# Optimization experiments

Hardware: AMD Instinct MI355X
Metric: run time of the kernel (lower is better)

## Reference

```python
import jax, jax.numpy as jnp
import numpy as np

N_CLASS = 20
N_SIGMA = 2
H = W = 512
B = 4
N_INST = 32
W_INST, W_VAR, W_SEED = 1.0, 10.0, 1.0
FG_WEIGHT = 10.0


def _xym():
    # channel 0: x along width, channel 1: y along height (matches torch buffer)
    xm = jnp.broadcast_to(jnp.linspace(0.0, 1.0, W)[None, :], (H, W))
    ym = jnp.broadcast_to(jnp.linspace(0.0, 1.0, H)[:, None], (H, W))
    return jnp.stack([xm, ym], axis=0)  # [2, H, W]


def lovasz_hinge_flat(logits, gt, valid):
    # logits, gt (0/1 float), valid (bool), all flat [P]; ignored pixels excluded
    P = logits.shape[0]
    vf = valid.astype(logits.dtype)
    signs = 2.0 * gt - 1.0
    # push ignored pixels to the end of the descending sort; relu(-1e9)=0 kills them
    errors = jnp.where(valid, 1.0 - logits * signs, -1e9)
    errors_sorted, perm = jax.lax.top_k(errors, P)  # descending
    gt_sorted = jnp.take(gt * vf, perm)
    v_sorted = jnp.take(vf, perm)
    gts = jnp.sum(gt * vf)
    inter = gts - jnp.cumsum(gt_sorted)
    union = gts + jnp.cumsum((1.0 - gt_sorted) * v_sorted)
    jac = 1.0 - inter / jnp.maximum(union, 1e-9)
    jac = jnp.concatenate([jac[:1], jac[1:] - jac[:-1]])
    return jnp.sum(jax.nn.relu(errors_sorted) * jac)


def _per_image(pred_b, inst_b, lab_b, xym, fg_w, n_inst):
    spatial_emb = jnp.tanh(pred_b[:2]) + xym            # [2,H,W]
    sigma = pred_b[2:2 + N_SIGMA]                       # [n_sigma,H,W]
    seed = jax.nn.sigmoid(pred_b[2 + N_SIGMA:2 + N_SIGMA + N_CLASS])  # [C,H,W]
    inst = inst_b[0]
    lab = lab_b[0]
    valid = (lab != 255)

    # background seed loss: sum over classes of seed^2 on pixels not of that class
    cls_ids = jnp.arange(N_CLASS)
    bg = (lab[None] != (cls_ids + 1)[:, None, None]) & valid[None]
    seed_bg = jnp.sum(jnp.square(seed) * bg)

    def per_inst(iid):
        m = (inst == iid)
        mf = m.astype(pred_b.dtype)
        cnt = jnp.maximum(jnp.sum(mf), 1.0)
        # to_center=True: center is mean coordinate of instance pixels
        center = jnp.sum(xym * mf[None], axis=(1, 2)) / cnt          # [2]
        s_mean = jnp.sum(sigma * mf[None], axis=(1, 2)) / cnt        # [n_sigma]
        var_l = jnp.sum(jnp.square(sigma - jax.lax.stop_gradient(s_mean)[:, None, None]) * mf[None]) / (N_SIGMA * cnt)
        s = jnp.exp(s_mean * 10.0)
        dist = jnp.exp(-jnp.sum(jnp.square(spatial_emb - center[:, None, None]) * s[:, None, None], axis=0))  # [H,W]
        inst_l = lovasz_hinge_flat((dist * 2.0 - 1.0).reshape(-1), mf.reshape(-1), valid.reshape(-1))
        cls = jnp.max(lab * m) - 1  # instance class (0-indexed)
        seed_c = jnp.take(seed, cls, axis=0)
        seed_fg = jnp.take(fg_w, cls) * jnp.sum(jnp.square(seed_c - jax.lax.stop_gradient(dist)) * mf)
        return inst_l, var_l, seed_fg

    inst_ls, var_ls, seed_fgs = jax.vmap(per_inst)(jnp.arange(1, n_inst + 1))
    instance_loss = jnp.sum(inst_ls) / n_inst
    var_loss = jnp.sum(var_ls) / n_inst
    seed_loss = (seed_bg + jnp.sum(seed_fgs)) / (H * W)
    return W_INST * instance_loss + W_VAR * var_loss + W_SEED * seed_loss


def setup_inputs() -> dict:
    key = jax.random.key(0)
    k1, k2 = jax.random.split(key)
    prediction = jax.random.normal(k1, (B, 2 + N_SIGMA + N_CLASS, H, W), dtype=jnp.float32)
    instances = jax.random.randint(k2, (B, 1, H, W), 0, N_INST + 1).astype(jnp.int32)
    # each instance id has a consistent class, as the torch instance_to_cls dict assumes
    labels = jnp.where(instances > 0, ((instances - 1) % N_CLASS) + 1, 0).astype(jnp.int32)
    return {"prediction": prediction, "instances": instances, "labels": labels, "n_instances": N_INST}


def reference(prediction, instances, labels, n_instances):
    xym = _xym()
    fg_w = jnp.full((N_CLASS,), FG_WEIGHT, dtype=prediction.dtype)
    per = jax.vmap(lambda p, i, l: _per_image(p, i, l, xym, fg_w, n_instances))(prediction, instances, labels)
    return jnp.mean(per) + jnp.sum(prediction) * 0.0
```

## Files before the change

kernel.cpp:

```cpp
#include <hip/hip_runtime.h>
#include <hip/hip_fp16.h>
#include <math.h>

#define HH 512
#define WW 512
#define BB 4
#define NCLS 20
#define NINST 32
#define NPIX (HH*WW)
#define NCH 24
#define NBIN 128
#define NCHUNK3 256
#define CPX3 1024
#define K3T 512
#define HSTR 33

#define OFF_PARTA  ((size_t)0)
#define OFF_PSEED  (OFF_PARTA + 1024*256*4)
#define OFF_STATS  (OFF_PSEED + 1024*8)
#define OFF_SEEDBG (OFF_STATS + 8*128*4)
#define OFF_VALID  (OFF_SEEDBG + 4*4)
#define OFF_INSTL  (OFF_VALID + 4*4)
#define OFF_SFG    (OFF_INSTL + 128*4)
#define OFF_REC    ((OFF_SFG + 1024*4 + 255) & ~(size_t)255)
#define OFF_HIST   (OFF_REC + (size_t)BB*NPIX*8)

__device__ __forceinline__ float fast_rcp(float x) { return __builtin_amdgcn_rcpf(x); }
__device__ __forceinline__ float fast_sigmoid(float z) { return fast_rcp(1.0f + __expf(-z)); }
__device__ __forceinline__ float fast_tanh(float x) {
  return 1.0f - 2.0f * fast_rcp(__expf(2.0f * x) + 1.0f);
}

__global__ __launch_bounds__(256) void k1_stats(
    const float* __restrict__ pred, const int* __restrict__ inst,
    const int* __restrict__ lab,
    float* __restrict__ partA, float2* __restrict__ partSeed,
    uint2* __restrict__ rec)
{
  __shared__ unsigned s_st[4][NINST][9];
  __shared__ float s_seed, s_valid;
  int t = threadIdx.x;
  int w = t >> 6;
  for (int i = t; i < 4*NINST*9; i += 256) ((unsigned*)s_st)[i] = 0u;
  if (t == 0) { s_seed = 0.f; s_valid = 0.f; }
  __syncthreads();

  int b = blockIdx.x >> 8;
  int p = (blockIdx.x & 255) * 1024 + t * 4;
  const float* pb = pred + (size_t)b*NCH*NPIX;

  float4 e0v = *(const float4*)(pb + p);
  float4 e1v = *(const float4*)(pb + NPIX + p);
  float4 g0v = *(const float4*)(pb + 2*NPIX + p);
  float4 g1v = *(const float4*)(pb + 3*NPIX + p);
  int4 idv = *(const int4*)(inst + (size_t)b*NPIX + p);
  int4 lbv = *(const int4*)(lab + (size_t)b*NPIX + p);
  float4 sv[12];
  #pragma unroll
  for (int c = 0; c < 12; ++c) sv[c] = *(const float4*)(pb + (size_t)(4+c)*NPIX + p);

  #pragma unroll
  for (int u = 0; u < 4; ++u) {
    int px = p + u;
    int x = px & (WW-1);
    int y = px >> 9;
    float xm = x * (1.0f/(WW-1));
    float ym = y * (1.0f/(HH-1));
    float g0 = (&g0v.x)[u];
    float g1 = (&g1v.x)[u];
    int id = (&idv.x)[u];
    int lb = (&lbv.x)[u];
    if (id >= 1) {
      int j = id - 1;
      unsigned* row = s_st[w][j];
      atomicAdd(&row[0], 1u | ((lb != 255) ? 0x10000u : 0u));
      atomicAdd((float*)&row[1], xm);
      atomicAdd((float*)&row[2], ym);
      atomicAdd((float*)&row[3], g0);
      atomicAdd((float*)&row[4], g1);
      atomicAdd((float*)&row[5], g0*g0);
      atomicAdd((float*)&row[6], g1*g1);
    }
  }

  float4 sv2[8];
  #pragma unroll
  for (int c = 0; c < 8; ++c) sv2[c] = *(const float4*)(pb + (size_t)(16+c)*NPIX + p);

  float so[4] = {0.f,0.f,0.f,0.f};
  float Sv[4] = {0.f,0.f,0.f,0.f};
  #pragma unroll
  for (int c = 0; c < 12; ++c) {
    #pragma unroll
    for (int u = 0; u < 4; ++u) {
      float sg = fast_sigmoid((&sv[c].x)[u]);
      Sv[u] += sg*sg;
      if (c + 1 == (&lbv.x)[u]) so[u] = sg;
    }
  }
  #pragma unroll
  for (int c = 0; c < 8; ++c) {
    #pragma unroll
    for (int u = 0; u < 4; ++u) {
      float sg = fast_sigmoid((&sv2[c].x)[u]);
      Sv[u] += sg*sg;
      if (c + 13 == (&lbv.x)[u]) so[u] = sg;
    }
  }
  float seedloc = 0.f, vloc = 0.f;
  #pragma unroll
  for (int u = 0; u < 4; ++u)
    if ((&lbv.x)[u] != 255) { seedloc += Sv[u] - so[u]*so[u]; vloc += 1.0f; }

  {
    uint2 r4[4];
    #pragma unroll
    for (int u = 0; u < 4; ++u) {
      int px = p + u;
      int x = px & (WW-1);
      int y = px >> 9;
      float ex = fast_tanh((&e0v.x)[u]) + x * (1.0f/(WW-1));
      float ey = fast_tanh((&e1v.x)[u]) + y * (1.0f/(HH-1));
      __half2 h = __floats2half2_rn(ex, ey);
      unsigned valid = ((&lbv.x)[u] != 255) ? 1u : 0u;
      unsigned meta = (unsigned)(&idv.x)[u] | (valid << 7);
      r4[u].x = *reinterpret_cast<unsigned*>(&h);
      r4[u].y = (unsigned)(unsigned char)(so[u]*255.f + 0.5f) | (meta << 8);
    }
    uint4* dst = (uint4*)(rec + (size_t)b*NPIX + p);
    dst[0] = make_uint4(r4[0].x, r4[0].y, r4[1].x, r4[1].y);
    dst[1] = make_uint4(r4[2].x, r4[2].y, r4[3].x, r4[3].y);
  }
  for (int o = 32; o; o >>= 1) {
    seedloc += __shfl_down(seedloc, o);
    vloc    += __shfl_down(vloc, o);
  }
  if ((t & 63) == 0) { atomicAdd(&s_seed, seedloc); atomicAdd(&s_valid, vloc); }
  __syncthreads();

  {
    int j = t & 31, f = t >> 5;
    float v;
    if (f == 0) {
      unsigned s = (s_st[0][j][0] & 0xFFFFu) + (s_st[1][j][0] & 0xFFFFu)
                 + (s_st[2][j][0] & 0xFFFFu) + (s_st[3][j][0] & 0xFFFFu);
      v = (float)s;
    } else if (f == 7) {
      unsigned s = (s_st[0][j][0] >> 16) + (s_st[1][j][0] >> 16)
                 + (s_st[2][j][0] >> 16) + (s_st[3][j][0] >> 16);
      v = (float)s;
    } else {
      v = __uint_as_float(s_st[0][j][f]) + __uint_as_float(s_st[1][j][f])
        + __uint_as_float(s_st[2][j][f]) + __uint_as_float(s_st[3][j][f]);
    }
    partA[(blockIdx.x << 8) + t] = v;
  }
  if (t == 0) partSeed[blockIdx.x] = make_float2(s_seed, s_valid);
}

__global__ __launch_bounds__(256) void k2a_reduce(
    const float* __restrict__ partA, const float2* __restrict__ partSeed,
    float* __restrict__ stats, float* __restrict__ seedbg,
    float* __restrict__ validT)
{
  int bid = blockIdx.x;
  int t = threadIdx.x;
  if (bid < 32) {
    __shared__ float red[256];
    int b = bid >> 3, f = bid & 7;
    int j = t & 31, grp = t >> 5;
    float s = 0.f;
    #pragma unroll 8
    for (int k = 0; k < 32; ++k)
      s += partA[((b*256 + grp*32 + k) << 8) + (f << 5) + j];
    red[t] = s; __syncthreads();
    for (int st = 128; st >= 32; st >>= 1) {
      if (t < st) red[t] += red[t + st];
      __syncthreads();
    }
    if (t < 32) stats[f*128 + b*32 + t] = red[t];
  } else {
    int img = t >> 6, slot = t & 63;
    float s = 0.f, v = 0.f;
    #pragma unroll
    for (int k = 0; k < 4; ++k) {
      float2 ps = partSeed[img*256 + slot*4 + k];
      s += ps.x; v += ps.y;
    }
    for (int o = 32; o; o >>= 1) {
      s += __shfl_down(s, o);
      v += __shfl_down(v, o);
    }
    if (slot == 0) { seedbg[img] = s; validT[img] = v; }
  }
}

__global__ __launch_bounds__(K3T) void k3_hist(
    const uint2* __restrict__ rec, const float* __restrict__ stats,
    unsigned* __restrict__ hist, float* __restrict__ sfg)
{
  __shared__ unsigned hc[NBIN*HSTR];
  __shared__ float sder[NINST][4];
  __shared__ float s_fg[8];
  int t = threadIdx.x;
  int bid = blockIdx.x;
  int b = bid >> 8;
  int chunk = bid & 255;
  for (int i = t; i < NBIN*HSTR; i += K3T) hc[i] = 0u;
  if (t < NINST) {
    int pr = b*NINST + t;
    float cnt = fmaxf(stats[0*128+pr], 1.0f);
    float rc = fast_rcp(cnt);
    sder[t][0] = stats[1*128+pr] * rc;
    sder[t][1] = stats[2*128+pr] * rc;
    sder[t][2] = -1.442695041f * __expf(10.f * stats[3*128+pr] * rc);
    sder[t][3] = -1.442695041f * __expf(10.f * stats[4*128+pr] * rc);
  }
  __syncthreads();

  int w = t >> 6, lane = t & 63;
  int j = lane & 31, jp1 = j + 1;
  float cx = sder[j][0], cy = sder[j][1];
  float s0 = sder[j][2], s1 = sder[j][3];
  const uint2* rb = rec + (size_t)b*NPIX + chunk*CPX3 + w*128;

  float fg = 0.f;
  #pragma unroll 4
  for (int r = 0; r < 64; ++r) {
    uint2 rv = rb[r*2 + (lane >> 5)];
    __half2 h;
    *reinterpret_cast<unsigned*>(&h) = rv.x;
    float2 e = __half22float2(h);
    unsigned hi = rv.y;
    float dx = e.x - cx, dy = e.y - cy;
    float dist = exp2f(dx*dx*s0 + dy*dy*s1);
    bool own = ((int)((hi >> 8) & 0x3F) == jp1);
    if (own) { float d = (float)(hi & 0xFFu)*(1.0f/255.f) - dist; fg += d*d; }
    if (hi & 0x8000u) {
      float f = own ? (1.0f - dist) : dist;
      unsigned bin = min((unsigned)(f * (float)NBIN), NBIN-1u);
      if (bin) atomicAdd(&hc[bin*HSTR + j], own ? 0x10001u : 1u);
    }
  }
  for (int o = 32; o; o >>= 1) fg += __shfl_down(fg, o);
  if (lane == 0) s_fg[w] = fg;
  __syncthreads();
  if (t == 0) {
    float s = 0.f;
    #pragma unroll
    for (int i = 0; i < 8; ++i) s += s_fg[i];
    sfg[bid] = 10.0f * s;
  }
  unsigned* out = hist + (size_t)(b*NCHUNK3 + chunk) * (NINST*NBIN);
  #pragma unroll
  for (int k = 0; k < NINST*NBIN/K3T; ++k) {
    int idx = k*K3T + t;
    out[idx] = hc[(idx & 127)*HSTR + (idx >> 7)];
  }
}

__global__ __launch_bounds__(512) void k4_scan(
    const unsigned* __restrict__ hist, const float* __restrict__ stats,
    const float* __restrict__ validT, float* __restrict__ instl)
{
  __shared__ unsigned s_c[4][NBIN], s_p[4][NBIN];
  __shared__ unsigned rc[NBIN], rp[NBIN];
  int t = threadIdx.x;
  int pair = blockIdx.x;
  int b = pair >> 5, j = pair & 31;
  int grp = t >> 7, bin = t & 127;
  const unsigned* bp = hist + ((size_t)b*NCHUNK3*NINST + j)*NBIN + bin;
  unsigned c = 0, p = 0;
  #pragma unroll 8
  for (int ch = grp*64; ch < grp*64 + 64; ++ch) {
    unsigned v = bp[(size_t)ch * (NINST*NBIN)];
    c += v & 0xFFFFu; p += v >> 16;
  }
  s_c[grp][bin] = c; s_p[grp][bin] = p;
  __syncthreads();
  if (t < NBIN) {
    unsigned cc = s_c[0][t] + s_c[1][t] + s_c[2][t] + s_c[3][t];
    unsigned pp = s_p[0][t] + s_p[1][t] + s_p[2][t] + s_p[3][t];
    s_c[0][t] = cc; s_p[0][t] = pp;
    rc[t] = t ? cc : 0u; rp[t] = t ? pp : 0u;
  }
  __syncthreads();
  for (int st = 64; st; st >>= 1) {
    if (t < st) { rc[t] += rc[t+st]; rp[t] += rp[t+st]; }
    __syncthreads();
  }
  float G = stats[7*128+pair];
  if (t == 0) {
    s_c[0][0] = (unsigned)validT[b] - rc[0];
    s_p[0][0] = (unsigned)G - rp[0];
  }
  __syncthreads();

  if (t < 64) {
    int lane = t;
    unsigned carryN = 0, carryP = 0;
    float Jprev = 0.f, L = 0.f;
    for (int c8 = 0; c8 < NBIN/64; ++c8) {
      int k = NBIN - 1 - c8*64 - lane;
      unsigned n = s_c[0][k], pp0 = s_p[0][k];
      for (int off = 1; off < 64; off <<= 1) {
        unsigned nn = __shfl_up(n, off);
        unsigned pq = __shfl_up(pp0, off);
        if (lane >= off) { n += nn; pp0 += pq; }
      }
      float fN = (float)(carryN + n);
      float fP = (float)(carryP + pp0);
      float uni = G + fN - fP;
      float J = 1.0f - (G - fP) / fmaxf(uni, 1e-9f);
      float Jp = __shfl_up(J, 1);
      if (lane == 0) Jp = Jprev;
      float v = (k + 0.5f) * (2.0f/NBIN);
      L += v * (J - Jp);
      carryN += __shfl(n, 63);
      carryP += __shfl(pp0, 63);
      Jprev  = __shfl(J, 63);
    }
    for (int o = 32; o; o >>= 1) L += __shfl_down(L, o);
    if (lane == 0) instl[pair] = L;
  }
}

__global__ __launch_bounds__(512) void k5_final(
    const float* __restrict__ instl, const float* __restrict__ stats,
    const float* __restrict__ seedbg, const float* __restrict__ sfg,
    float* __restrict__ out)
{
  __shared__ float red[512];
  int t = threadIdx.x;
  float acc = (sfg[t] + sfg[t + 512]) * (1.0f/NPIX);
  if (t < 4) acc += seedbg[t] * (1.0f/NPIX);
  if (t < 128) {
    float cntA = stats[0*128+t];
    float cnt = fmaxf(cntA, 1.0f);
    float s0 = stats[3*128+t], s1 = stats[4*128+t];
    float q0 = stats[5*128+t], q1 = stats[6*128+t];
    float sm0 = s0/cnt, sm1 = s1/cnt;
    float varnum = q0 - 2.f*sm0*s0 + cntA*sm0*sm0
                 + q1 - 2.f*sm1*s1 + cntA*sm1*sm1;
    float varl = varnum / (2.0f * cnt);
    acc += (instl[t] + 10.0f*varl) * (1.0f/NINST);
  }
  red[t] = acc; __syncthreads();
  for (int st = 256; st; st >>= 1) {
    if (t < st) red[t] += red[t+st];
    __syncthreads();
  }
  if (t == 0) out[0] = red[0] * (1.0f/BB);
}

extern "C" void kernel_launch(void* const* d_in, const int* in_sizes, int n_in,
                              void* d_out, int out_size, void* d_ws, size_t ws_size,
                              hipStream_t stream)
{
  const float* pred = (const float*)d_in[0];
  const int* inst = (const int*)d_in[1];
  const int* lab  = (const int*)d_in[2];
  char* ws = (char*)d_ws;
  float* partA = (float*)(ws + OFF_PARTA);
  float2* partSeed = (float2*)(ws + OFF_PSEED);
  float* stats = (float*)(ws + OFF_STATS);
  float* seedbg = (float*)(ws + OFF_SEEDBG);
  float* validT = (float*)(ws + OFF_VALID);
  float* instl = (float*)(ws + OFF_INSTL);
  float* sfg = (float*)(ws + OFF_SFG);
  uint2* rec = (uint2*)(ws + OFF_REC);
  unsigned* hist = (unsigned*)(ws + OFF_HIST);

  hipLaunchKernelGGL(k1_stats, dim3(1024), dim3(256), 0, stream,
                     pred, inst, lab, partA, partSeed, rec);
  hipLaunchKernelGGL(k2a_reduce, dim3(33), dim3(256), 0, stream,
                     partA, partSeed, stats, seedbg, validT);
  hipLaunchKernelGGL(k3_hist, dim3(BB*NCHUNK3), dim3(K3T), 0, stream,
                     rec, stats, hist, sfg);
  hipLaunchKernelGGL(k4_scan, dim3(128), dim3(512), 0, stream,
                     hist, stats, validT, instl);
  hipLaunchKernelGGL(k5_final, dim3(1), dim3(512), 0, stream,
                     instl, stats, seedbg, sfg, (float*)d_out);
}
```

Measured before the change: 91.79 us.

## Halve per-thread pixels in stats kernel and fuse final reduction into scan

The stats kernel now launches 2048 blocks with two pixels per thread instead of 1024 blocks with four. Seed channels are streamed in a loop rather than held as 20 float4 registers, which lowers register pressure and raises occupancy. The final single-block kernel is removed: each scan block adds its instance and variance terms to the output atomically, and block 0 also adds the seed terms. The output is zeroed in the first kernel, and float atomic accumulation makes the summation order nondeterministic.

New measurement: 89.05 us. -3.0%, faster.

```diff
diff --git a/kernel.cpp b/kernel.cpp
--- a/kernel.cpp
+++ b/kernel.cpp
@@ -16,12 +16,11 @@
 #define HSTR 33
 
 #define OFF_PARTA  ((size_t)0)
-#define OFF_PSEED  (OFF_PARTA + 1024*256*4)
-#define OFF_STATS  (OFF_PSEED + 1024*8)
+#define OFF_PSEED  (OFF_PARTA + 2048*256*4)
+#define OFF_STATS  (OFF_PSEED + 2048*8)
 #define OFF_SEEDBG (OFF_STATS + 8*128*4)
 #define OFF_VALID  (OFF_SEEDBG + 4*4)
-#define OFF_INSTL  (OFF_VALID + 4*4)
-#define OFF_SFG    (OFF_INSTL + 128*4)
+#define OFF_SFG    (OFF_VALID + 4*4)
 #define OFF_REC    ((OFF_SFG + 1024*4 + 255) & ~(size_t)255)
 #define OFF_HIST   (OFF_REC + (size_t)BB*NPIX*8)
 
@@ -35,7 +34,7 @@
     const float* __restrict__ pred, const int* __restrict__ inst,
     const int* __restrict__ lab,
     float* __restrict__ partA, float2* __restrict__ partSeed,
-    uint2* __restrict__ rec)
+    uint2* __restrict__ rec, float* __restrict__ outz)
 {
   __shared__ unsigned s_st[4][NINST][9];
   __shared__ float s_seed, s_valid;
@@ -43,24 +42,21 @@
   int w = t >> 6;
   for (int i = t; i < 4*NINST*9; i += 256) ((unsigned*)s_st)[i] = 0u;
   if (t == 0) { s_seed = 0.f; s_valid = 0.f; }
-  __syncthreads();
-
-  int b = blockIdx.x >> 8;
-  int p = (blockIdx.x & 255) * 1024 + t * 4;
+  if (blockIdx.x == 0 && t == 0) outz[0] = 0.f;
+  __syncthreads();
+
+  int b = blockIdx.x >> 9;
+  int p = (blockIdx.x & 511) * 512 + t * 2;
   const float* pb = pred + (size_t)b*NCH*NPIX;
-
-  float4 e0v = *(const float4*)(pb + p);
-  float4 e1v = *(const float4*)(pb + NPIX + p);
-  float4 g0v = *(const float4*)(pb + 2*NPIX + p);
-  float4 g1v = *(const float4*)(pb + 3*NPIX + p);
-  int4 idv = *(const int4*)(inst + (size_t)b*NPIX + p);
-  int4 lbv = *(const int4*)(lab + (size_t)b*NPIX + p);
-  float4 sv[12];
+  float2 e0v = *(const float2*)(pb + p);
+  float2 e1v = *(const float2*)(pb + NPIX + p);
+  float2 g0v = *(const float2*)(pb + 2*NPIX + p);
+  float2 g1v = *(const float2*)(pb + 3*NPIX + p);
+  int2 idv = *(const int2*)(inst + (size_t)b*NPIX + p);
+  int2 lbv = *(const int2*)(lab + (size_t)b*NPIX + p);
+
   #pragma unroll
-  for (int c = 0; c < 12; ++c) sv[c] = *(const float4*)(pb + (size_t)(4+c)*NPIX + p);
-
-  #pragma unroll
-  for (int u = 0; u < 4; ++u) {
+  for (int u = 0; u < 2; ++u) {
     int px = p + u;
     int x = px & (WW-1);
     int y = px >> 9;
@@ -83,53 +79,37 @@
     }
   }
 
-  float4 sv2[8];
-  #pragma unroll
-  for (int c = 0; c < 8; ++c) sv2[c] = *(const float4*)(pb + (size_t)(16+c)*NPIX + p);
-
-  float so[4] = {0.f,0.f,0.f,0.f};
-  float Sv[4] = {0.f,0.f,0.f,0.f};
-  #pragma unroll
-  for (int c = 0; c < 12; ++c) {
+  float so0 = 0.f, so1 = 0.f, Sv0 = 0.f, Sv1 = 0.f;
+  for (int c = 0; c < NCLS; ++c) {
+    float2 sv = *(const float2*)(pb + (size_t)(4+c)*NPIX + p);
+    float sg0 = fast_sigmoid(sv.x);
+    float sg1 = fast_sigmoid(sv.y);
+    Sv0 += sg0*sg0;
+    Sv1 += sg1*sg1;
+    if (c + 1 == lbv.x) so0 = sg0;
+    if (c + 1 == lbv.y) so1 = sg1;
+  }
+  float seedloc = 0.f, vloc = 0.f;
+  if (lbv.x != 255) { seedloc += Sv0 - so0*so0; vloc += 1.0f; }
+  if (lbv.y != 255) { seedloc += Sv1 - so1*so1; vloc += 1.0f; }
+
+  {
+    uint2 r4[2];
     #pragma unroll
-    for (int u = 0; u < 4; ++u) {
-      float sg = fast_sigmoid((&sv[c].x)[u]);
-      Sv[u] += sg*sg;
-      if (c + 1 == (&lbv.x)[u]) so[u] = sg;
-    }
-  }
-  #pragma unroll
-  for (int c = 0; c < 8; ++c) {
-    #pragma unroll
-    for (int u = 0; u < 4; ++u) {
-      float sg = fast_sigmoid((&sv2[c].x)[u]);
-      Sv[u] += sg*sg;
-      if (c + 13 == (&lbv.x)[u]) so[u] = sg;
-    }
-  }
-  float seedloc = 0.f, vloc = 0.f;
-  #pragma unroll
-  for (int u = 0; u < 4; ++u)
-    if ((&lbv.x)[u] != 255) { seedloc += Sv[u] - so[u]*so[u]; vloc += 1.0f; }
-
-  {
-    uint2 r4[4];
-    #pragma unroll
-    for (int u = 0; u < 4; ++u) {
+    for (int u = 0; u < 2; ++u) {
       int px = p + u;
       int x = px & (WW-1);
       int y = px >> 9;
       float ex = fast_tanh((&e0v.x)[u]) + x * (1.0f/(WW-1));
       float ey = fast_tanh((&e1v.x)[u]) + y * (1.0f/(HH-1));
       __half2 h = __floats2half2_rn(ex, ey);
-      unsigned valid = ((&lbv.x)[u] != 255) ? 1u : 0u;
+      unsigned valid = (((&lbv.x)[u]) != 255) ? 1u : 0u;
       unsigned meta = (unsigned)(&idv.x)[u] | (valid << 7);
+      float sou = u ? so1 : so0;
       r4[u].x = *reinterpret_cast<unsigned*>(&h);
-      r4[u].y = (unsigned)(unsigned char)(so[u]*255.f + 0.5f) | (meta << 8);
-    }
-    uint4* dst = (uint4*)(rec + (size_t)b*NPIX + p);
-    dst[0] = make_uint4(r4[0].x, r4[0].y, r4[1].x, r4[1].y);
-    dst[1] = make_uint4(r4[2].x, r4[2].y, r4[3].x, r4[3].y);
+      r4[u].y = (unsigned)(unsigned char)(sou*255.f + 0.5f) | (meta << 8);
+    }
+    *(uint4*)(rec + (size_t)b*NPIX + p) = make_uint4(r4[0].x, r4[0].y, r4[1].x, r4[1].y);
   }
   for (int o = 32; o; o >>= 1) {
     seedloc += __shfl_down(seedloc, o);
@@ -171,8 +151,8 @@
     int j = t & 31, grp = t >> 5;
     float s = 0.f;
     #pragma unroll 8
-    for (int k = 0; k < 32; ++k)
-      s += partA[((b*256 + grp*32 + k) << 8) + (f << 5) + j];
+    for (int k = 0; k < 64; ++k)
+      s += partA[((b*512 + grp*64 + k) << 8) + (f << 5) + j];
     red[t] = s; __syncthreads();
     for (int st = 128; st >= 32; st >>= 1) {
       if (t < st) red[t] += red[t + st];
@@ -183,8 +163,8 @@
     int img = t >> 6, slot = t & 63;
     float s = 0.f, v = 0.f;
     #pragma unroll
-    for (int k = 0; k < 4; ++k) {
-      float2 ps = partSeed[img*256 + slot*4 + k];
+    for (int k = 0; k < 8; ++k) {
+      float2 ps = partSeed[img*512 + slot*8 + k];
       s += ps.x; v += ps.y;
     }
     for (int o = 32; o; o >>= 1) {
@@ -259,12 +239,14 @@
   }
 }
 
-__global__ __launch_bounds__(512) void k4_scan(
+__global__ __launch_bounds__(512) void k4_final(
     const unsigned* __restrict__ hist, const float* __restrict__ stats,
-    const float* __restrict__ validT, float* __restrict__ instl)
+    const float* __restrict__ validT, const float* __restrict__ seedbg,
+    const float* __restrict__ sfg, float* __restrict__ out)
 {
   __shared__ unsigned s_c[4][NBIN], s_p[4][NBIN];
   __shared__ unsigned rc[NBIN], rp[NBIN];
+  __shared__ float s_L;
   int t = threadIdx.x;
   int pair = blockIdx.x;
   int b = pair >> 5, j = pair & 31;
@@ -321,36 +303,31 @@
       Jprev  = __shfl(J, 63);
     }
     for (int o = 32; o; o >>= 1) L += __shfl_down(L, o);
-    if (lane == 0) instl[pair] = L;
-  }
-}
-
-__global__ __launch_bounds__(512) void k5_final(
-    const float* __restrict__ instl, const float* __restrict__ stats,
-    const float* __restrict__ seedbg, const float* __restrict__ sfg,
-    float* __restrict__ out)
-{
-  __shared__ float red[512];
-  int t = threadIdx.x;
-  float acc = (sfg[t] + sfg[t + 512]) * (1.0f/NPIX);
-  if (t < 4) acc += seedbg[t] * (1.0f/NPIX);
-  if (t < 128) {
-    float cntA = stats[0*128+t];
+    if (lane == 0) s_L = L;
+  }
+  __syncthreads();
+  if (t == 0) {
+    float cntA = stats[0*128+pair];
     float cnt = fmaxf(cntA, 1.0f);
-    float s0 = stats[3*128+t], s1 = stats[4*128+t];
-    float q0 = stats[5*128+t], q1 = stats[6*128+t];
+    float s0 = stats[3*128+pair], s1 = stats[4*128+pair];
+    float q0 = stats[5*128+pair], q1 = stats[6*128+pair];
     float sm0 = s0/cnt, sm1 = s1/cnt;
     float varnum = q0 - 2.f*sm0*s0 + cntA*sm0*sm0
                  + q1 - 2.f*sm1*s1 + cntA*sm1*sm1;
     float varl = varnum / (2.0f * cnt);
-    acc += (instl[t] + 10.0f*varl) * (1.0f/NINST);
-  }
-  red[t] = acc; __syncthreads();
-  for (int st = 256; st; st >>= 1) {
-    if (t < st) red[t] += red[t+st];
-    __syncthreads();
-  }
-  if (t == 0) out[0] = red[0] * (1.0f/BB);
+    atomicAdd(out, (s_L + 10.0f*varl) * (1.0f/(NINST*BB)));
+  }
+  if (pair == 0) {
+    __shared__ float red[512];
+    float acc = sfg[t] + sfg[t + 512];
+    if (t < 4) acc += seedbg[t];
+    red[t] = acc; __syncthreads();
+    for (int st = 256; st; st >>= 1) {
+      if (t < st) red[t] += red[t+st];
+      __syncthreads();
+    }
+    if (t == 0) atomicAdd(out, red[0] * (1.0f/((float)NPIX*BB)));
+  }
 }
 
 extern "C" void kernel_launch(void* const* d_in, const int* in_sizes, int n_in,
@@ -366,19 +343,16 @@
   float* stats = (float*)(ws + OFF_STATS);
   float* seedbg = (float*)(ws + OFF_SEEDBG);
   float* validT = (float*)(ws + OFF_VALID);
-  float* instl = (float*)(ws + OFF_INSTL);
   float* sfg = (float*)(ws + OFF_SFG);
   uint2* rec = (uint2*)(ws + OFF_REC);
   unsigned* hist = (unsigned*)(ws + OFF_HIST);
 
-  hipLaunchKernelGGL(k1_stats, dim3(1024), dim3(256), 0, stream,
-                     pred, inst, lab, partA, partSeed, rec);
+  hipLaunchKernelGGL(k1_stats, dim3(2048), dim3(256), 0, stream,
+                     pred, inst, lab, partA, partSeed, rec, (float*)d_out);
   hipLaunchKernelGGL(k2a_reduce, dim3(33), dim3(256), 0, stream,
                      partA, partSeed, stats, seedbg, validT);
   hipLaunchKernelGGL(k3_hist, dim3(BB*NCHUNK3), dim3(K3T), 0, stream,
                      rec, stats, hist, sfg);
-  hipLaunchKernelGGL(k4_scan, dim3(128), dim3(512), 0, stream,
-                     hist, stats, validT, instl);
-  hipLaunchKernelGGL(k5_final, dim3(1), dim3(512), 0, stream,
-                     instl, stats, seedbg, sfg, (float*)d_out);
-}
+  hipLaunchKernelGGL(k4_final, dim3(128), dim3(512), 0, stream,
+                     hist, stats, validT, seedbg, sfg, (float*)d_out);
+}
```
